# Kernel optimization log

Measured on AMD Instinct MI355X. Metric: run time of the kernel, lower is better.

## Reference

```python
import jax, jax.numpy as jnp
import numpy as np
import math

NUM_BUCKETS = 32
MAX_DISTANCE = 128
N_HEADS = 16
D_KV = 64


def _relative_position_bucket(relative_position, num_buckets=NUM_BUCKETS, max_distance=MAX_DISTANCE):
    # bidirectional (encoder) variant: is_decoder=False
    nb = num_buckets // 2
    rel_buckets = (relative_position > 0).astype(jnp.int32) * nb
    rp = jnp.abs(relative_position)
    max_exact = nb // 2
    is_small = rp < max_exact
    rp_large = max_exact + (
        jnp.log(rp.astype(jnp.float32) / max_exact)
        / math.log(max_distance / max_exact)
        * (nb - max_exact)
    ).astype(jnp.int32)
    rp_large = jnp.minimum(rp_large, nb - 1)
    return rel_buckets + jnp.where(is_small, rp, rp_large)


def compute_position_bias(rel_bias_table, q_len, k_len):
    ctx = jnp.arange(q_len, dtype=jnp.int32)[:, None]
    mem = jnp.arange(k_len, dtype=jnp.int32)[None, :]
    buckets = _relative_position_bucket(mem - ctx)  # [q_len, k_len]
    values = rel_bias_table[buckets]                # [q_len, k_len, H]
    return jnp.transpose(values, (2, 0, 1))[None]   # [1, H, q_len, k_len]


def setup_inputs() -> dict:
    key = jax.random.key(0)
    ks = jax.random.split(key, 6)
    B, S, D = 2, 2048, 1024
    s = 0.02
    return {
        "hidden_states": jax.random.normal(ks[0], (B, S, D), dtype=jnp.float32),
        "Wq": jax.random.normal(ks[1], (D, N_HEADS * D_KV), dtype=jnp.float32) * s,
        "Wk": jax.random.normal(ks[2], (D, N_HEADS * D_KV), dtype=jnp.float32) * s,
        "Wv": jax.random.normal(ks[3], (D, N_HEADS * D_KV), dtype=jnp.float32) * s,
        "Wo": jax.random.normal(ks[4], (N_HEADS * D_KV, D), dtype=jnp.float32) * s,
        "rel_bias_table": jax.random.normal(ks[5], (NUM_BUCKETS, N_HEADS), dtype=jnp.float32),
    }


def reference(hidden_states, Wq, Wk, Wv, Wo, rel_bias_table):
    B, S, D = hidden_states.shape
    H, dh = N_HEADS, D_KV
    q = (hidden_states @ Wq).reshape(B, S, H, dh)
    k = (hidden_states @ Wk).reshape(B, S, H, dh)
    v = (hidden_states @ Wv).reshape(B, S, H, dh)

    position_bias = compute_position_bias(rel_bias_table, S, S)  # [1,H,S,S]

    scale = 1.0 / math.sqrt(dh)  # applied inside optimized_attention (SDPA convention)
    scores = jnp.einsum('bqhd,bkhd->bhqk', q, k) * scale + position_bias
    probs = jax.nn.softmax(scores, axis=-1)
    ctx = jnp.einsum('bhqk,bkhd->bqhd', probs, v).reshape(B, S, H * dh)
    attn_output = ctx @ Wo
    return attn_output
```

## Files before the change

### kernel.cpp

```cpp
#include <hip/hip_runtime.h>

typedef __attribute__((ext_vector_type(8))) short s16x8;
typedef __attribute__((ext_vector_type(4))) short s16x4;
typedef __attribute__((ext_vector_type(4))) float f32x4;
typedef __attribute__((ext_vector_type(4))) unsigned int u32x4;
typedef __attribute__((ext_vector_type(2))) unsigned int u32x2;
typedef unsigned short u16;
typedef unsigned int u32;

#define LOG2E 1.4426950408889634f

__device__ __forceinline__ u16 f2bf(float x) {
  u32 u = __float_as_uint(x);
  u += 0x7FFFu + ((u >> 16) & 1u);
  return (u16)(u >> 16);
}

__device__ __forceinline__ float bf2f(u16 x) {
  return __uint_as_float((u32)x << 16);
}

__device__ __forceinline__ u32 pack_bf_trunc(float lo, float hi) {
  return __builtin_amdgcn_perm(__float_as_uint(hi), __float_as_uint(lo), 0x07060302u);
}

__device__ __forceinline__ void gl_lds16(const void* g, void* l) {
  __builtin_amdgcn_global_load_lds((const __attribute__((address_space(1))) void*)g,
                                   (__attribute__((address_space(3))) void*)l, 16, 0, 0);
}

#define MFMA16(a, b, c) __builtin_amdgcn_mfma_f32_16x16x32_bf16((a), (b), (c), 0, 0, 0)


__global__ __launch_bounds__(256) void prep(const float* __restrict__ hs,
                                            const float* __restrict__ Wq,
                                            const float* __restrict__ Wk,
                                            const float* __restrict__ Wv,
                                            const float* __restrict__ Wo,
                                            const float* __restrict__ tbl,
                                            u16* __restrict__ hsb,
                                            u16* __restrict__ wt,
                                            u16* __restrict__ wot,
                                            float* __restrict__ biasT) {
  const int blk = blockIdx.x;
  const int tid = threadIdx.x;
  if (blk < 2048) {
    const int i = blk * 256 + tid;
    const float4* s4 = (const float4*)hs;
    float4 a = s4[i * 2];
    float4 b = s4[i * 2 + 1];
    s16x8 o;
    o[0] = (short)f2bf(a.x); o[1] = (short)f2bf(a.y);
    o[2] = (short)f2bf(a.z); o[3] = (short)f2bf(a.w);
    o[4] = (short)f2bf(b.x); o[5] = (short)f2bf(b.y);
    o[6] = (short)f2bf(b.z); o[7] = (short)f2bf(b.w);
    *(s16x8*)&hsb[i * 8] = o;
  } else if (blk < 4096) {
    int r = blk - 2048;
    const int sel = r >> 9;
    r &= 511;
    const float* W = sel == 0 ? Wq : (sel == 1 ? Wk : (sel == 2 ? Wv : Wo));
    u16* dst = sel == 3 ? wot : wt + sel * 1048576;
    const int n = (r & 15) * 64 + (tid & 63);
    const int kb = (r >> 4) * 32 + (tid >> 6) * 8;
    s16x8 o;
#pragma unroll
    for (int j = 0; j < 8; ++j) o[j] = (short)f2bf(W[(kb + j) * 1024 + n]);
    *(s16x8*)&dst[n * 1024 + kb] = o;
  } else {
    const int i = (blk - 4096) * 256 + tid;
    const int h = i >> 12, dp = i & 4095;
    const int delta = dp - 2047;
    const int rp = delta < 0 ? -delta : delta;
    int bucket = delta > 0 ? 16 : 0;
    if (rp < 8)
      bucket += rp;
    else
      bucket += 8 + (rp >= 12) + (rp >= 16) + (rp >= 23) + (rp >= 32) +
                (rp >= 46) + (rp >= 64) + (rp >= 91);
    biasT[i] = tbl[bucket * 16 + h] * LOG2E;
  }
}


__device__ __forceinline__ void gemm_core(const u16* __restrict__ A,
                                          const u16* __restrict__ Bt,
                                          int m0, int n0,
                                          u16* shbuf, f32x4 acc[4][4]) {
  const int tid = threadIdx.x;
  const int w = tid >> 6, l = tid & 63, g = l >> 4, m15 = l & 15;
  const int wr = (w >> 1) * 64, wc = (w & 1) * 64;
#pragma unroll
  for (int i = 0; i < 4; ++i)
#pragma unroll
    for (int j = 0; j < 4; ++j) acc[i][j] = (f32x4){0.f, 0.f, 0.f, 0.f};

#define GSTAGE(buf, k0)                                                    \
  {                                                                        \
    _Pragma("unroll") for (int c = 0; c < 2; ++c) {                        \
      const int idx = c * 256 + tid;                                       \
      const int row = idx >> 2, col4 = idx & 3;                            \
      const int scol = col4 ^ ((row >> 1) & 3);                            \
      gl_lds16(&A[(m0 + row) * 1024 + (k0) + scol * 8],                    \
               (char*)shbuf + (buf)*8192 + c * 4096 + w * 1024);           \
      gl_lds16(&Bt[(n0 + row) * 1024 + (k0) + scol * 8],                   \
               (char*)shbuf + 16384 + (buf)*8192 + c * 4096 + w * 1024);   \
    }                                                                      \
  }

  GSTAGE(0, 0);
  int cur = 0;
  for (int kt = 0; kt < 32; ++kt) {
    __syncthreads();
    if (kt < 31) GSTAGE(cur ^ 1, (kt + 1) * 32);
    const u16* Asb = shbuf + cur * 4096;
    const u16* Bsb = shbuf + 8192 + cur * 4096;
    s16x8 af[4], bfr[4];
#pragma unroll
    for (int mf = 0; mf < 4; ++mf) {
      const int row = wr + mf * 16 + m15;
      af[mf] = *(const s16x8*)&Asb[(row * 4 + (g ^ ((row >> 1) & 3))) * 8];
    }
#pragma unroll
    for (int nf = 0; nf < 4; ++nf) {
      const int row = wc + nf * 16 + m15;
      bfr[nf] = *(const s16x8*)&Bsb[(row * 4 + (g ^ ((row >> 1) & 3))) * 8];
    }
#pragma unroll
    for (int mf = 0; mf < 4; ++mf)
#pragma unroll
      for (int nf = 0; nf < 4; ++nf)
        acc[mf][nf] = MFMA16(af[mf], bfr[nf], acc[mf][nf]);
    cur ^= 1;
  }
#undef GSTAGE
}

__global__ __launch_bounds__(256) void gemm_qkv(const u16* __restrict__ X,
                                                const u16* __restrict__ Wt,
                                                u16* __restrict__ Q,
                                                u16* __restrict__ Kb,
                                                u16* __restrict__ VT) {
  __shared__ u16 shbuf[16384];
  f32x4 acc[4][4];
  const int flat = blockIdx.x;
  const int x = flat & 7, i = flat >> 3;
  const int m0 = ((x & 3) * 8 + (i & 7)) * 128;
  const int n0 = ((x >> 2) * 12 + (i >> 3)) * 128;
  gemm_core(X, Wt, m0, n0, shbuf, acc);

  const int tid = threadIdx.x;
  const int w = tid >> 6, l = tid & 63, g = l >> 4, m15 = l & 15;
  const int wr = (w >> 1) * 64, wc = (w & 1) * 64;
  const int nsel = n0 >> 10;
  const int ncol0 = (n0 & 1023) + wc;
  if (nsel == 2) {
    __syncthreads();
#pragma unroll
    for (int mf = 0; mf < 4; ++mf) {
      const int s_base = wr + mf * 16 + g * 4;
#pragma unroll
      for (int nf = 0; nf < 4; ++nf) {
        const int d_loc = wc + nf * 16 + m15;
        s16x4 pk;
#pragma unroll
        for (int r = 0; r < 4; ++r) pk[r] = (short)f2bf(acc[mf][nf][r]);
        *(s16x4*)&shbuf[d_loc * 128 + (s_base ^ ((d_loc & 7) << 3))] = pk;
      }
    }
    __syncthreads();
    const int b = m0 >> 11, sg0 = m0 & 2047;
#pragma unroll
    for (int it = 0; it < 8; ++it) {
      const int d_loc = it * 16 + w * 4 + g;
      const s16x8 v =
          *(const s16x8*)&shbuf[d_loc * 128 + ((m15 * 8) ^ ((d_loc & 7) << 3))];
      const int col = (n0 & 1023) + d_loc;
      *(s16x8*)&VT[((b * 16 + (col >> 6)) * 64 + (col & 63)) * 2048 + sg0 + m15 * 8] = v;
    }
  } else {
    u16* dst = nsel == 0 ? Q : Kb;
    const float scale = nsel == 0 ? 0.125f * LOG2E : 1.0f;
#pragma unroll
    for (int mf = 0; mf < 4; ++mf) {
      const int rbase = m0 + wr + mf * 16 + g * 4;
#pragma unroll
      for (int nf = 0; nf < 4; ++nf) {
        const int col = ncol0 + nf * 16 + m15;
#pragma unroll
        for (int r = 0; r < 4; ++r)
          dst[(rbase + r) * 1024 + col] = f2bf(acc[mf][nf][r] * scale);
      }
    }
  }
}


__global__ __launch_bounds__(256) void gemm_out(const u16* __restrict__ CTX,
                                                const u16* __restrict__ Wot,
                                                float* __restrict__ Out) {
  __shared__ u16 shbuf[12288];
  f32x4 acc[4][2];
  const int flat = blockIdx.x;
  const int x = flat & 7, i = flat >> 3;
  const int m0 = ((x & 3) * 8 + (i & 7)) * 128;
  const int n0 = ((x >> 2) * 8 + (i >> 3)) * 64;

  const int tid = threadIdx.x;
  const int w = tid >> 6, l = tid & 63, g = l >> 4, m15 = l & 15;
  const int wr = (w >> 1) * 64, wc = (w & 1) * 32;
#pragma unroll
  for (int mf = 0; mf < 4; ++mf)
#pragma unroll
    for (int nf = 0; nf < 2; ++nf) acc[mf][nf] = (f32x4){0.f, 0.f, 0.f, 0.f};

#define OSTAGE(buf, k0)                                                    \
  {                                                                        \
    _Pragma("unroll") for (int c = 0; c < 2; ++c) {                        \
      const int idx = c * 256 + tid;                                       \
      const int row = idx >> 2, col4 = idx & 3;                            \
      const int scol = col4 ^ ((row >> 1) & 3);                            \
      gl_lds16(&CTX[(m0 + row) * 1024 + (k0) + scol * 8],                  \
               (char*)shbuf + (buf)*8192 + c * 4096 + w * 1024);           \
    }                                                                      \
    {                                                                      \
      const int row = tid >> 2, col4 = tid & 3;                            \
      const int scol = col4 ^ ((row >> 1) & 3);                            \
      gl_lds16(&Wot[(n0 + row) * 1024 + (k0) + scol * 8],                  \
               (char*)shbuf + 16384 + (buf)*4096 + (w >> 1) * 2048 +       \
                   (tid & 127) * 16);                                      \
    }                                                                      \
  }

  OSTAGE(0, 0);
  int cur = 0;
  for (int kt = 0; kt < 32; ++kt) {
    __syncthreads();
    if (kt < 31) OSTAGE(cur ^ 1, (kt + 1) * 32);
    const u16* Asb = shbuf + cur * 4096;
    const u16* Bsb = shbuf + 8192 + cur * 2048;
    s16x8 af[4], bfr[2];
#pragma unroll
    for (int mf = 0; mf < 4; ++mf) {
      const int row = wr + mf * 16 + m15;
      af[mf] = *(const s16x8*)&Asb[(row * 4 + (g ^ ((row >> 1) & 3))) * 8];
    }
#pragma unroll
    for (int nf = 0; nf < 2; ++nf) {
      const int row = wc + nf * 16 + m15;
      bfr[nf] = *(const s16x8*)&Bsb[(row * 4 + (g ^ ((row >> 1) & 3))) * 8];
    }
#pragma unroll
    for (int mf = 0; mf < 4; ++mf)
#pragma unroll
      for (int nf = 0; nf < 2; ++nf)
        acc[mf][nf] = MFMA16(af[mf], bfr[nf], acc[mf][nf]);
    cur ^= 1;
  }
#undef OSTAGE

#pragma unroll
  for (int mf = 0; mf < 4; ++mf) {
    const int rbase = m0 + wr + mf * 16 + g * 4;
#pragma unroll
    for (int nf = 0; nf < 2; ++nf) {
      const int col = n0 + wc + nf * 16 + m15;
#pragma unroll
      for (int r = 0; r < 4; ++r)
        Out[(rbase + r) * 1024 + col] = acc[mf][nf][r];
    }
  }
}


__global__ __launch_bounds__(256, 4) void attn_kernel(const u16* __restrict__ Qg,
                                                      const u16* __restrict__ Kg,
                                                      const u16* __restrict__ VTg,
                                                      const float* __restrict__ biasT,
                                                      const float* __restrict__ tbl,
                                                      u16* __restrict__ po0,
                                                      u16* __restrict__ po1,
                                                      float* __restrict__ pls) {
  __shared__ u16 KT[2][4096];
  __shared__ u16 VTs[2][4096];

  const int tid = threadIdx.x;
  const int w = tid >> 6, l = tid & 63, g = l >> 4, m15 = l & 15;
  const int flat = blockIdx.x;
  const int nf_ = (flat & 7) * 128 + (flat >> 3);
  const int bh = nf_ >> 5;
  const int rem = nf_ & 31;
  const int half = rem >> 4, qblk = rem & 15;
  const int b = bh >> 4, h = bh & 15;
  const int qw = qblk * 128 + w * 32;
  const int kvbase = half * 1024;

  u16* poh = half ? po1 : po0;
  float* plsh = pls + half * 65536;

  const float fpos = tbl[31 * 16 + h] * LOG2E;
  const float fneg = tbl[15 * 16 + h] * LOG2E;

  s16x8 aq[2][2];
#pragma unroll
  for (int qs = 0; qs < 2; ++qs) {
    const u16* qp = &Qg[(b * 2048 + qw + qs * 16 + m15) * 1024 + h * 64 + g * 8];
    aq[qs][0] = *(const s16x8*)qp;
    aq[qs][1] = *(const s16x8*)(qp + 32);
  }

  s16x8 vone;
#pragma unroll
  for (int j = 0; j < 8; ++j) vone[j] = (short)0x3F80;

  f32x4 o[2][4];
  f32x4 ls4[2];
#pragma unroll
  for (int qs = 0; qs < 2; ++qs) {
    ls4[qs] = (f32x4){0.f, 0.f, 0.f, 0.f};
#pragma unroll
    for (int d = 0; d < 4; ++d) o[qs][d] = (f32x4){0.f, 0.f, 0.f, 0.f};
  }

  const u16* Kbase = &Kg[(b * 2048 + kvbase) * 1024 + h * 64];
  const u16* Vbase = &VTg[bh * 64 * 2048 + kvbase];

#define STAGE(buf, kv0)                                                          \
  {                                                                              \
    _Pragma("unroll") for (int c = 0; c < 2; ++c) {                              \
      const int idx = c * 256 + tid;                                             \
      const int row = idx >> 3, col16 = idx & 7;                                 \
      const int scol = col16 ^ (row & 7);                                        \
      gl_lds16(&Kbase[(kv0 + row) * 1024 + scol * 8],                            \
               (char*)KT + (buf)*8192 + c * 4096 + w * 1024);                    \
      gl_lds16(&Vbase[row * 2048 + (kv0) + scol * 8],                            \
               (char*)VTs + (buf)*8192 + c * 4096 + w * 1024);                   \
    }                                                                            \
  }

  STAGE(0, 0);
  int cur = 0;
  for (int t = 0; t < 16; ++t) {
    const int kv0 = t * 64;
    __syncthreads();
    if (t < 15) STAGE(cur ^ 1, kv0 + 64);

    const u16* KTc = &KT[cur][0];
    const u16* VTc = &VTs[cur][0];

    f32x4 s[2][4];
    const int diff = kvbase + kv0 - qw;
    if (diff <= -160 || diff >= 128) {
      const float bc = diff > 0 ? fpos : fneg;
#pragma unroll
      for (int qs = 0; qs < 2; ++qs)
#pragma unroll
        for (int c = 0; c < 4; ++c) s[qs][c] = (f32x4){bc, bc, bc, bc};
    } else {
#pragma unroll
      for (int qs = 0; qs < 2; ++qs) {
        const float* bp =
            &biasT[h * 4096 + kvbase + kv0 + g * 4 - qw - qs * 16 - m15 + 2047];
#pragma unroll
        for (int c = 0; c < 4; ++c)
#pragma unroll
          for (int r = 0; r < 4; ++r) s[qs][c][r] = bp[c * 16 + r];
      }
    }

    __builtin_amdgcn_s_setprio(1);
#pragma unroll
    for (int ks = 0; ks < 2; ++ks) {
#pragma unroll
      for (int c = 0; c < 4; ++c) {
        const int row = c * 16 + m15;
        const s16x8 bk = *(const s16x8*)&KTc[(row * 8 + ((ks * 4 + g) ^ (row & 7))) * 8];
        s[0][c] = MFMA16(bk, aq[0][ks], s[0][c]);
        s[1][c] = MFMA16(bk, aq[1][ks], s[1][c]);
      }
    }
    __builtin_amdgcn_s_setprio(0);

    s16x8 pa[2][2];
#pragma unroll
    for (int qs = 0; qs < 2; ++qs) {
      u32 w01[4], w23[4];
#pragma unroll
      for (int c = 0; c < 4; ++c) {
        w01[c] = pack_bf_trunc(__builtin_amdgcn_exp2f(s[qs][c][0]),
                               __builtin_amdgcn_exp2f(s[qs][c][1]));
        w23[c] = pack_bf_trunc(__builtin_amdgcn_exp2f(s[qs][c][2]),
                               __builtin_amdgcn_exp2f(s[qs][c][3]));
      }
#pragma unroll
      for (int ks = 0; ks < 2; ++ks) {
        u32x2 rA = __builtin_amdgcn_permlane32_swap(w01[2 * ks], w01[2 * ks + 1], false, false);
        u32x2 rB = __builtin_amdgcn_permlane16_swap(rA[0], rA[1], false, false);
        u32x2 rC = __builtin_amdgcn_permlane32_swap(w23[2 * ks], w23[2 * ks + 1], false, false);
        u32x2 rD = __builtin_amdgcn_permlane16_swap(rC[0], rC[1], false, false);
        const u32x4 pd = (u32x4){rB[0], rD[0], rB[1], rD[1]};
        pa[qs][ks] = __builtin_bit_cast(s16x8, pd);
      }
    }

    __builtin_amdgcn_s_setprio(1);
#pragma unroll
    for (int ks = 0; ks < 2; ++ks) {
#pragma unroll
      for (int d = 0; d < 4; ++d) {
        const int rowv = d * 16 + m15;
        const s16x8 bv = *(const s16x8*)&VTc[(rowv * 8 + ((ks * 4 + g) ^ (rowv & 7))) * 8];
        o[0][d] = MFMA16(pa[0][ks], bv, o[0][d]);
        o[1][d] = MFMA16(pa[1][ks], bv, o[1][d]);
      }
      ls4[0] = MFMA16(pa[0][ks], vone, ls4[0]);
      ls4[1] = MFMA16(pa[1][ks], vone, ls4[1]);
    }
    __builtin_amdgcn_s_setprio(0);
    cur ^= 1;
  }
#undef STAGE

#pragma unroll
  for (int qs = 0; qs < 2; ++qs) {
    const int orow = b * 2048 + qw + qs * 16 + g * 4;
    const int ocol = h * 64 + m15;
#pragma unroll
    for (int r = 0; r < 4; ++r) {
#pragma unroll
      for (int d = 0; d < 4; ++d)
        poh[(orow + r) * 1024 + ocol + d * 16] = f2bf(o[qs][d][r]);
      if (m15 == 0) plsh[(orow + r) * 16 + h] = ls4[qs][r];
    }
  }
}

__global__ __launch_bounds__(256) void merge(const u16* __restrict__ po0,
                                             const u16* __restrict__ po1,
                                             const float* __restrict__ pls,
                                             u16* __restrict__ ctx) {
  const int i = blockIdx.x * 256 + threadIdx.x;
  const int row = i >> 7;
  const int seg = i & 127;
  const int h = seg >> 3;
  const float den = 1.0f / (pls[row * 16 + h] + pls[65536 + row * 16 + h]);
  const s16x8 a = *(const s16x8*)&po0[row * 1024 + seg * 8];
  const s16x8 b = *(const s16x8*)&po1[row * 1024 + seg * 8];
  s16x8 o;
#pragma unroll
  for (int j = 0; j < 8; ++j)
    o[j] = (short)f2bf((bf2f((u16)a[j]) + bf2f((u16)b[j])) * den);
  *(s16x8*)&ctx[row * 1024 + seg * 8] = o;
}


extern "C" void kernel_launch(void* const* d_in, const int* in_sizes, int n_in,
                              void* d_out, int out_size, void* d_ws, size_t ws_size,
                              hipStream_t stream) {
  (void)in_sizes; (void)n_in; (void)out_size; (void)ws_size;
  const float* hs  = (const float*)d_in[0];
  const float* Wq  = (const float*)d_in[1];
  const float* Wk  = (const float*)d_in[2];
  const float* Wv  = (const float*)d_in[3];
  const float* Wo  = (const float*)d_in[4];
  const float* tbl = (const float*)d_in[5];

  char* ws = (char*)d_ws;
  u16* hsb   = (u16*)(ws);
  u16* wt    = (u16*)(ws + 8388608);
  u16* wot   = (u16*)(ws + 14680064);
  u16* q     = (u16*)(ws + 16777216);
  u16* k     = (u16*)(ws + 25165824);
  u16* po0   = (u16*)(ws + 33554432);
  u16* vt    = (u16*)(ws + 41943040);
  u16* ctx   = (u16*)(ws + 50331648);
  float* biasT = (float*)(ws + 58720256);
  u16* po1   = hsb;
  float* pls = (float*)wt;

  prep<<<4352, 256, 0, stream>>>(hs, Wq, Wk, Wv, Wo, tbl, hsb, wt, wot, biasT);
  gemm_qkv<<<768, 256, 0, stream>>>(hsb, wt, q, k, vt);
  attn_kernel<<<1024, 256, 0, stream>>>(q, k, vt, biasT, tbl, po0, po1, pls);
  merge<<<2048, 256, 0, stream>>>(po0, po1, pls, ctx);
  gemm_out<<<512, 256, 0, stream>>>(ctx, wot, (float*)d_out);
}
```

Measured before the change: 117.3 us.

## Fuse split-KV merge into output projection GEMM A-tile loading

Removes the separate merge kernel and instead combines the two partial attention outputs and normalises them by the summed softmax denominators while staging the A tile inside gemm_out. This eliminates the ctx buffer write and re-read and one kernel launch. In exchange, gemm_out reads two bf16 partial buffers through registers instead of using direct global-to-LDS copies, adding ALU work and register-staged latency inside the GEMM loop.

```diff
diff --git a/kernel.cpp b/kernel.cpp
--- a/kernel.cpp
+++ b/kernel.cpp
@@ -196,10 +196,13 @@
 }
 
 
-__global__ __launch_bounds__(256) void gemm_out(const u16* __restrict__ CTX,
+__global__ __launch_bounds__(256) void gemm_out(const u16* __restrict__ po0,
+                                                const u16* __restrict__ po1,
+                                                const float* __restrict__ pls,
                                                 const u16* __restrict__ Wot,
                                                 float* __restrict__ Out) {
   __shared__ u16 shbuf[12288];
+  __shared__ float denbuf[2048];
   f32x4 acc[4][2];
   const int flat = blockIdx.x;
   const int x = flat & 7, i = flat >> 3;
@@ -214,29 +217,69 @@
 #pragma unroll
     for (int nf = 0; nf < 2; ++nf) acc[mf][nf] = (f32x4){0.f, 0.f, 0.f, 0.f};
 
-#define OSTAGE(buf, k0)                                                    \
+  for (int jj = tid; jj < 2048; jj += 256) {
+    const int li = (m0 + (jj >> 4)) * 16 + (jj & 15);
+    denbuf[jj] = 1.0f / (pls[li] + pls[65536 + li]);
+  }
+
+  int arow[2], acol[2], adst[2];
+#pragma unroll
+  for (int c = 0; c < 2; ++c) {
+    const int idx = c * 256 + tid;
+    const int row = idx >> 2, col4 = idx & 3;
+    arow[c] = row;
+    acol[c] = (col4 ^ ((row >> 1) & 3)) * 8;
+    adst[c] = (row * 4 + col4) * 8;
+  }
+
+  s16x8 la[2], lb[2];
+
+#define A_LOAD(k0)                                                         \
   {                                                                        \
     _Pragma("unroll") for (int c = 0; c < 2; ++c) {                        \
-      const int idx = c * 256 + tid;                                       \
-      const int row = idx >> 2, col4 = idx & 3;                            \
-      const int scol = col4 ^ ((row >> 1) & 3);                            \
-      gl_lds16(&CTX[(m0 + row) * 1024 + (k0) + scol * 8],                  \
-               (char*)shbuf + (buf)*8192 + c * 4096 + w * 1024);           \
+      const int off = (m0 + arow[c]) * 1024 + (k0) + acol[c];              \
+      la[c] = *(const s16x8*)&po0[off];                                    \
+      lb[c] = *(const s16x8*)&po1[off];                                    \
     }                                                                      \
-    {                                                                      \
-      const int row = tid >> 2, col4 = tid & 3;                            \
-      const int scol = col4 ^ ((row >> 1) & 3);                            \
-      gl_lds16(&Wot[(n0 + row) * 1024 + (k0) + scol * 8],                  \
-               (char*)shbuf + 16384 + (buf)*4096 + (w >> 1) * 2048 +       \
-                   (tid & 127) * 16);                                      \
-    }                                                                      \
-  }
-
-  OSTAGE(0, 0);
+  }
+
+#define A_WRITE(buf, k0)                                                         \
+  {                                                                              \
+    _Pragma("unroll") for (int c = 0; c < 2; ++c) {                              \
+      const float den = denbuf[arow[c] * 16 + (((k0) + acol[c]) >> 6)];          \
+      u32 pk[4];                                                                 \
+      _Pragma("unroll") for (int j = 0; j < 4; ++j) {                            \
+        const float v0 =                                                         \
+            (bf2f((u16)la[c][2 * j]) + bf2f((u16)lb[c][2 * j])) * den;           \
+        const float v1 =                                                         \
+            (bf2f((u16)la[c][2 * j + 1]) + bf2f((u16)lb[c][2 * j + 1])) * den;   \
+        pk[j] = pack_bf_trunc(v0, v1);                                           \
+      }                                                                          \
+      *(u32x4*)&shbuf[(buf)*4096 + adst[c]] = (u32x4){pk[0], pk[1], pk[2], pk[3]}; \
+    }                                                                            \
+  }
+
+#define B_STAGE(buf, k0)                                                   \
+  {                                                                        \
+    const int row = tid >> 2, col4 = tid & 3;                              \
+    const int scol = col4 ^ ((row >> 1) & 3);                              \
+    gl_lds16(&Wot[(n0 + row) * 1024 + (k0) + scol * 8],                    \
+             (char*)shbuf + 16384 + (buf)*4096 + (w >> 1) * 2048 +         \
+                 (tid & 127) * 16);                                        \
+  }
+
+  A_LOAD(0);
+  B_STAGE(0, 0);
+  __syncthreads();
+  A_WRITE(0, 0);
+
   int cur = 0;
   for (int kt = 0; kt < 32; ++kt) {
     __syncthreads();
-    if (kt < 31) OSTAGE(cur ^ 1, (kt + 1) * 32);
+    if (kt < 31) {
+      A_LOAD((kt + 1) * 32);
+      B_STAGE(cur ^ 1, (kt + 1) * 32);
+    }
     const u16* Asb = shbuf + cur * 4096;
     const u16* Bsb = shbuf + 8192 + cur * 2048;
     s16x8 af[4], bfr[2];
@@ -255,9 +298,12 @@
 #pragma unroll
       for (int nf = 0; nf < 2; ++nf)
         acc[mf][nf] = MFMA16(af[mf], bfr[nf], acc[mf][nf]);
+    if (kt < 31) A_WRITE(cur ^ 1, (kt + 1) * 32);
     cur ^= 1;
   }
-#undef OSTAGE
+#undef A_LOAD
+#undef A_WRITE
+#undef B_STAGE
 
 #pragma unroll
   for (int mf = 0; mf < 4; ++mf) {
@@ -435,24 +481,6 @@
   }
 }
 
-__global__ __launch_bounds__(256) void merge(const u16* __restrict__ po0,
-                                             const u16* __restrict__ po1,
-                                             const float* __restrict__ pls,
-                                             u16* __restrict__ ctx) {
-  const int i = blockIdx.x * 256 + threadIdx.x;
-  const int row = i >> 7;
-  const int seg = i & 127;
-  const int h = seg >> 3;
-  const float den = 1.0f / (pls[row * 16 + h] + pls[65536 + row * 16 + h]);
-  const s16x8 a = *(const s16x8*)&po0[row * 1024 + seg * 8];
-  const s16x8 b = *(const s16x8*)&po1[row * 1024 + seg * 8];
-  s16x8 o;
-#pragma unroll
-  for (int j = 0; j < 8; ++j)
-    o[j] = (short)f2bf((bf2f((u16)a[j]) + bf2f((u16)b[j])) * den);
-  *(s16x8*)&ctx[row * 1024 + seg * 8] = o;
-}
-
 
 extern "C" void kernel_launch(void* const* d_in, const int* in_sizes, int n_in,
                               void* d_out, int out_size, void* d_ws, size_t ws_size,
@@ -473,7 +501,6 @@
   u16* k     = (u16*)(ws + 25165824);
   u16* po0   = (u16*)(ws + 33554432);
   u16* vt    = (u16*)(ws + 41943040);
-  u16* ctx   = (u16*)(ws + 50331648);
   float* biasT = (float*)(ws + 58720256);
   u16* po1   = hsb;
   float* pls = (float*)wt;
@@ -481,6 +508,5 @@
   prep<<<4352, 256, 0, stream>>>(hs, Wq, Wk, Wv, Wo, tbl, hsb, wt, wot, biasT);
   gemm_qkv<<<768, 256, 0, stream>>>(hsb, wt, q, k, vt);
   attn_kernel<<<1024, 256, 0, stream>>>(q, k, vt, biasT, tbl, po0, po1, pls);
-  merge<<<2048, 256, 0, stream>>>(po0, po1, pls, ctx);
-  gemm_out<<<512, 256, 0, stream>>>(ctx, wot, (float*)d_out);
-}
+  gemm_out<<<512, 256, 0, stream>>>(po0, po1, pls, wot, (float*)d_out);
+}
```

Result: slower. 126.5 us (+7.8%).
